# Optimization experiments

Hardware: AMD Instinct MI355X
Metric: run time of the kernel (lower is better)

The kernel has to match this reference:

```python
import jax, jax.numpy as jnp
import numpy as np

DROP_SCALE = 1e-4  # tf.multiply(feat_dropout, 0.0001)


def setup_inputs() -> dict:
    key = jax.random.key(0)
    k1, k2 = jax.random.split(key)
    B, C, N, D = 128, 2, 256, 256
    x = jax.random.normal(k1, (B, C, N, D), dtype=jnp.float32)
    # glorot_uniform for kernel [C*N*D, N]
    fan_in, fan_out = C * N * D, N
    limit = np.sqrt(6.0 / (fan_in + fan_out)).astype(np.float32)
    W = jax.random.uniform(k2, (fan_in, fan_out), dtype=jnp.float32,
                           minval=-limit, maxval=limit)
    return {"x": x, "W": W}


def _forward(x, W):
    B, C, N, D = x.shape
    K = N // 2  # with continuous data, exactly half strictly exceed the median
    # Keras Flatten(channels_first): permute to channels-last order, then flatten
    xf = jnp.transpose(x, (0, 2, 3, 1)).reshape(B, -1)          # [B, N*D*C]
    line = jax.nn.sigmoid(xf @ W)                                # [B, N]
    med = jnp.median(line, axis=-1, keepdims=True)               # [B, 1]
    mask = med < line                                            # [B, N] bool
    mask3 = jnp.broadcast_to(mask[:, None, :], (B, C, N))        # tile over channels
    # ragged boolean_mask + to_tensor == stable compaction of kept rows.
    # Stable argsort of (~mask) puts True (kept) positions first, in order.
    idx_att = jnp.argsort(~mask3, axis=-1, stable=True)[..., :K]   # [B, C, K]
    idx_drp = jnp.argsort(mask3, axis=-1, stable=True)[..., :K]    # [B, C, K]
    feat_att = jnp.take_along_axis(x, idx_att[..., None], axis=2)  # [B, C, K, D]
    feat_drp = jnp.take_along_axis(x, idx_drp[..., None], axis=2)  # [B, C, K, D]
    return feat_att + DROP_SCALE * feat_drp


def reference(x, W):
    return _forward(x, W)
```

## Files before the change

### kernel.cpp

```cpp
#include <hip/hip_runtime.h>

#define BATCH 128
#define CH    2
#define NN    256
#define DD    256
#define KTOT  131072
#define KHALF 128

#define KSPLIT 256
#define KLEN   (KTOT / KSPLIT)
#define KS     32
#define NSTAGE (KLEN / KS)
#define NTB    128
#define PITCH  40

typedef short bf16x8 __attribute__((ext_vector_type(8)));
typedef float f32x4  __attribute__((ext_vector_type(4)));

__device__ __forceinline__ unsigned short bf16_rne(float f) {
    unsigned int u = __float_as_uint(f);
    u += 0x7FFFu + ((u >> 16) & 1u);
    return (unsigned short)(u >> 16);
}
__device__ __forceinline__ float bf16f(unsigned short h) {
    return __uint_as_float(((unsigned int)h) << 16);
}
__device__ __forceinline__ uint4 pack8(const unsigned short* p) {
    uint4 r;
    r.x = (unsigned)p[0] | ((unsigned)p[1] << 16);
    r.y = (unsigned)p[2] | ((unsigned)p[3] << 16);
    r.z = (unsigned)p[4] | ((unsigned)p[5] << 16);
    r.w = (unsigned)p[6] | ((unsigned)p[7] << 16);
    return r;
}

template <bool ATOMIC>
__global__ __launch_bounds__(256, 2) void gemm_mfma(const float* __restrict__ x,
                                                    const float* __restrict__ W,
                                                    float* __restrict__ zout) {
    __shared__ unsigned short Ah[128][PITCH], Al[128][PITCH];
    __shared__ unsigned short Bh[NTB][PITCH], Bl[NTB][PITCH];

    const int bid = blockIdx.x;
    const int s   = ((bid >> 4) << 3) | (bid & 7);
    const int nh  = (bid >> 3) & 1;

    const int t  = threadIdx.x;
    const int k0 = s * KLEN;
    const int c  = k0 >> 16;
    const int nd_base = k0 & 65535;

    const int ra = t & 127;
    const int ha = t >> 7;
    const int cb = t & 127;
    const int hb = t >> 7;

    float av[16], bv[16];

    auto load_stage = [&](int st) {
        const float* xp = &x[(size_t)ra * KTOT + k0 + st * KS + 16 * ha];
        *(float4*)&av[0]  = *(const float4*)&xp[0];
        *(float4*)&av[4]  = *(const float4*)&xp[4];
        *(float4*)&av[8]  = *(const float4*)&xp[8];
        *(float4*)&av[12] = *(const float4*)&xp[12];
        const int nd0 = nd_base + st * KS + 16 * hb;
        const float* wp = &W[(size_t)(2 * nd0 + c) * NN + nh * NTB + cb];
#pragma unroll
        for (int i = 0; i < 16; ++i)
            bv[i] = wp[(size_t)i * 2 * NN];
    };

    auto write_stage = [&]() {
        unsigned short h[16], l[16];
#pragma unroll
        for (int i = 0; i < 16; ++i) {
            h[i] = bf16_rne(av[i]);
            l[i] = bf16_rne(av[i] - bf16f(h[i]));
        }
        *(uint4*)&Ah[ra][16 * ha]     = pack8(h);
        *(uint4*)&Ah[ra][16 * ha + 8] = pack8(h + 8);
        *(uint4*)&Al[ra][16 * ha]     = pack8(l);
        *(uint4*)&Al[ra][16 * ha + 8] = pack8(l + 8);
#pragma unroll
        for (int i = 0; i < 16; ++i) {
            h[i] = bf16_rne(bv[i]);
            l[i] = bf16_rne(bv[i] - bf16f(h[i]));
        }
        *(uint4*)&Bh[cb][16 * hb]     = pack8(h);
        *(uint4*)&Bh[cb][16 * hb + 8] = pack8(h + 8);
        *(uint4*)&Bl[cb][16 * hb]     = pack8(l);
        *(uint4*)&Bl[cb][16 * hb + 8] = pack8(l + 8);
    };

    const int lane = t & 63;
    const int wid  = t >> 6;
    const int wm   = (wid >> 1) * 64;
    const int wn   = (wid & 1) * 64;
    const int lr   = lane & 15;
    const int kq   = (lane >> 4) * 8;

    f32x4 acc[4][4] = {};

    auto compute_stage = [&]() {
        bf16x8 a_h[4], a_l[4];
#pragma unroll
        for (int mt = 0; mt < 4; ++mt) {
            a_h[mt] = *(const bf16x8*)&Ah[wm + mt * 16 + lr][kq];
            a_l[mt] = *(const bf16x8*)&Al[wm + mt * 16 + lr][kq];
        }
#pragma unroll
        for (int nt = 0; nt < 4; ++nt) {
            bf16x8 b_h = *(const bf16x8*)&Bh[wn + nt * 16 + lr][kq];
            bf16x8 b_l = *(const bf16x8*)&Bl[wn + nt * 16 + lr][kq];
#pragma unroll
            for (int mt = 0; mt < 4; ++mt) {
                acc[mt][nt] = __builtin_amdgcn_mfma_f32_16x16x32_bf16(a_h[mt], b_h, acc[mt][nt], 0, 0, 0);
                acc[mt][nt] = __builtin_amdgcn_mfma_f32_16x16x32_bf16(a_h[mt], b_l, acc[mt][nt], 0, 0, 0);
                acc[mt][nt] = __builtin_amdgcn_mfma_f32_16x16x32_bf16(a_l[mt], b_h, acc[mt][nt], 0, 0, 0);
            }
        }
    };

    load_stage(0);
    for (int st = 0; st < NSTAGE; ++st) {
        __syncthreads();
        write_stage();
        __syncthreads();
        if (st + 1 < NSTAGE) load_stage(st + 1);
        compute_stage();
    }

#pragma unroll
    for (int mt = 0; mt < 4; ++mt)
#pragma unroll
        for (int nt = 0; nt < 4; ++nt)
#pragma unroll
            for (int r = 0; r < 4; ++r) {
                const int row = wm + mt * 16 + (lane >> 4) * 4 + r;
                const int col = nh * NTB + wn + nt * 16 + lr;
                if (ATOMIC) atomicAdd(&zout[row * NN + col], acc[mt][nt][r]);
                else zout[(size_t)s * (BATCH * NN) + row * NN + col] = acc[mt][nt][r];
            }
}

__global__ __launch_bounds__(256) void reduce1(const float* __restrict__ part,
                                               float* __restrict__ part2) {
    const int g = blockIdx.x & 7;
    const int b = blockIdx.x >> 3;
    const int j = threadIdx.x;
    float v = 0.0f;
#pragma unroll
    for (int i = 0; i < 32; ++i)
        v += part[(size_t)(g * 32 + i) * (BATCH * NN) + b * NN + j];
    part2[(size_t)g * (BATCH * NN) + b * NN + j] = v;
}

__global__ __launch_bounds__(256) void select_kernel(const float* __restrict__ p2, int ngroups,
                                                     int* __restrict__ idx_att,
                                                     int* __restrict__ idx_drp) {
    __shared__ float zv[NN];
    __shared__ int   flags[NN];
    const int b = blockIdx.x;
    const int j = threadIdx.x;
    float v = 0.0f;
    for (int g = 0; g < ngroups; ++g)
        v += p2[(size_t)g * (BATCH * NN) + b * NN + j];
    zv[j] = v;
    __syncthreads();
    int rank = 0;
    for (int i = 0; i < NN; ++i) {
        const float u = zv[i];
        rank += (u < v) || (u == v && i < j);
    }
    const int kept = (rank >= KHALF) ? 1 : 0;
    flags[j] = kept;
    __syncthreads();
    int pos = 0;
    for (int i = 0; i < j; ++i) pos += flags[i];
    if (kept) idx_att[b * KHALF + pos]       = j;
    else      idx_drp[b * KHALF + (j - pos)] = j;
}

__global__ __launch_bounds__(256) void gather_kernel(const float* __restrict__ x,
                                                     const int* __restrict__ idx_att,
                                                     const int* __restrict__ idx_drp,
                                                     float* __restrict__ out) {
    const int row  = blockIdx.x * 4 + (threadIdx.x >> 6);
    const int lane = threadIdx.x & 63;
    const int k = row & 127;
    const int c = (row >> 7) & 1;
    const int b = row >> 8;
    const int ia = idx_att[b * KHALF + k];
    const int id = idx_drp[b * KHALF + k];
    const float4* pa = (const float4*)&x[((b * 2 + c) * NN + ia) * DD];
    const float4* pd = (const float4*)&x[((b * 2 + c) * NN + id) * DD];
    float4* po = (float4*)&out[(size_t)row * DD];
    const float4 a  = pa[lane];
    const float4 d4 = pd[lane];
    float4 o;
    o.x = a.x + 1e-4f * d4.x;
    o.y = a.y + 1e-4f * d4.y;
    o.z = a.z + 1e-4f * d4.z;
    o.w = a.w + 1e-4f * d4.w;
    po[lane] = o;
}

extern "C" void kernel_launch(void* const* d_in, const int* in_sizes, int n_in,
                              void* d_out, int out_size, void* d_ws, size_t ws_size,
                              hipStream_t stream) {
    const float* x = (const float*)d_in[0];
    const float* W = (const float*)d_in[1];
    float* out = (float*)d_out;

    const size_t part_bytes  = (size_t)KSPLIT * BATCH * NN * sizeof(float);
    const size_t part2_bytes = (size_t)8 * BATCH * NN * sizeof(float);
    const size_t idx_bytes   = (size_t)BATCH * KHALF * sizeof(int);

    if (ws_size >= part_bytes + part2_bytes + 2 * idx_bytes) {
        float* part    = (float*)d_ws;
        float* part2   = (float*)((char*)d_ws + part_bytes);
        int*   idx_att = (int*)((char*)d_ws + part_bytes + part2_bytes);
        int*   idx_drp = idx_att + BATCH * KHALF;
        gemm_mfma<false><<<512, 256, 0, stream>>>(x, W, part);
        reduce1<<<1024, 256, 0, stream>>>(part, part2);
        select_kernel<<<BATCH, 256, 0, stream>>>(part2, 8, idx_att, idx_drp);
        gather_kernel<<<BATCH * CH * KHALF / 4, 256, 0, stream>>>(x, idx_att, idx_drp, out);
    } else {
        float* z       = (float*)d_ws;
        int*   idx_att = (int*)((char*)d_ws + (size_t)BATCH * NN * sizeof(float));
        int*   idx_drp = idx_att + BATCH * KHALF;
        hipMemsetAsync(z, 0, (size_t)BATCH * NN * sizeof(float), stream);
        gemm_mfma<true><<<512, 256, 0, stream>>>(x, W, z);
        select_kernel<<<BATCH, 256, 0, stream>>>(z, 1, idx_att, idx_drp);
        gather_kernel<<<BATCH * CH * KHALF / 4, 256, 0, stream>>>(x, idx_att, idx_drp, out);
    }
}
```

Measured before the change: 274.6 us.

## Double split-K slices, double-buffer register prefetch, and use bf16 intrinsics

Templates the split-K GEMM on slice count and launches 512 slices (1024 blocks) when the workspace is large enough, keeping a 256-slice fallback. It adds a two-register-set prefetch with an unrolled stage loop so the next stage's global load is issued earlier. It also remaps block indices so neighbouring blocks take different slices, and uses packed bf16 conversion intrinsics for the hi/lo split. The extra parallelism costs twice the partial-sum traffic and more reduction work, and the two register sets raise register pressure.

```diff
diff --git a/kernel.cpp b/kernel.cpp
--- a/kernel.cpp
+++ b/kernel.cpp
@@ -1,4 +1,5 @@
 #include <hip/hip_runtime.h>
+#include <hip/hip_bf16.h>
 
 #define BATCH 128
 #define CH    2
@@ -7,43 +8,37 @@
 #define KTOT  131072
 #define KHALF 128
 
-#define KSPLIT 256
-#define KLEN   (KTOT / KSPLIT)
-#define KS     32
-#define NSTAGE (KLEN / KS)
-#define NTB    128
-#define PITCH  40
+#define KS    32
+#define NTB   128
+#define PITCH 40
 
 typedef short bf16x8 __attribute__((ext_vector_type(8)));
 typedef float f32x4  __attribute__((ext_vector_type(4)));
 
-__device__ __forceinline__ unsigned short bf16_rne(float f) {
-    unsigned int u = __float_as_uint(f);
-    u += 0x7FFFu + ((u >> 16) & 1u);
-    return (unsigned short)(u >> 16);
-}
-__device__ __forceinline__ float bf16f(unsigned short h) {
-    return __uint_as_float(((unsigned int)h) << 16);
-}
-__device__ __forceinline__ uint4 pack8(const unsigned short* p) {
-    uint4 r;
-    r.x = (unsigned)p[0] | ((unsigned)p[1] << 16);
-    r.y = (unsigned)p[2] | ((unsigned)p[3] << 16);
-    r.z = (unsigned)p[4] | ((unsigned)p[5] << 16);
-    r.w = (unsigned)p[6] | ((unsigned)p[7] << 16);
-    return r;
-}
-
-template <bool ATOMIC>
+__device__ __forceinline__ void hilo2(float a, float b, unsigned& hp, unsigned& lp) {
+    union { __hip_bfloat162 v; unsigned u; } H, L;
+    H.v = __float22bfloat162_rn(float2{a, b});
+    hp = H.u;
+    float2 hf = __bfloat1622float2(H.v);
+    L.v = __float22bfloat162_rn(float2{a - hf.x, b - hf.y});
+    lp = L.u;
+}
+
+template <int SLICES, bool ATOMIC>
 __global__ __launch_bounds__(256, 2) void gemm_mfma(const float* __restrict__ x,
                                                     const float* __restrict__ W,
                                                     float* __restrict__ zout) {
+    constexpr int KLEN = KTOT / SLICES;
+    constexpr int NST  = KLEN / KS;
+    constexpr int NBLK = SLICES * 2;
+
     __shared__ unsigned short Ah[128][PITCH], Al[128][PITCH];
     __shared__ unsigned short Bh[NTB][PITCH], Bl[NTB][PITCH];
 
-    const int bid = blockIdx.x;
-    const int s   = ((bid >> 4) << 3) | (bid & 7);
-    const int nh  = (bid >> 3) & 1;
+    const int bid     = blockIdx.x;
+    const int logical = (bid & 7) * (NBLK >> 3) + (bid >> 3);
+    const int s       = logical >> 1;
+    const int nh      = logical & 1;
 
     const int t  = threadIdx.x;
     const int k0 = s * KLEN;
@@ -55,41 +50,39 @@
     const int cb = t & 127;
     const int hb = t >> 7;
 
-    float av[16], bv[16];
-
-    auto load_stage = [&](int st) {
-        const float* xp = &x[(size_t)ra * KTOT + k0 + st * KS + 16 * ha];
+    const float* xrow = &x[(size_t)ra * KTOT + k0 + 16 * ha];
+    const float* wcol = &W[(size_t)(2 * (nd_base + 16 * hb) + c) * NN + nh * NTB + cb];
+
+    auto loadr = [&](float* av, float* bv, int st) {
+        const float* xp = xrow + st * KS;
         *(float4*)&av[0]  = *(const float4*)&xp[0];
         *(float4*)&av[4]  = *(const float4*)&xp[4];
         *(float4*)&av[8]  = *(const float4*)&xp[8];
         *(float4*)&av[12] = *(const float4*)&xp[12];
-        const int nd0 = nd_base + st * KS + 16 * hb;
-        const float* wp = &W[(size_t)(2 * nd0 + c) * NN + nh * NTB + cb];
+        const float* wp = wcol + (size_t)st * KS * 2 * NN;
 #pragma unroll
         for (int i = 0; i < 16; ++i)
             bv[i] = wp[(size_t)i * 2 * NN];
     };
 
-    auto write_stage = [&]() {
-        unsigned short h[16], l[16];
-#pragma unroll
-        for (int i = 0; i < 16; ++i) {
-            h[i] = bf16_rne(av[i]);
-            l[i] = bf16_rne(av[i] - bf16f(h[i]));
-        }
-        *(uint4*)&Ah[ra][16 * ha]     = pack8(h);
-        *(uint4*)&Ah[ra][16 * ha + 8] = pack8(h + 8);
-        *(uint4*)&Al[ra][16 * ha]     = pack8(l);
-        *(uint4*)&Al[ra][16 * ha + 8] = pack8(l + 8);
-#pragma unroll
-        for (int i = 0; i < 16; ++i) {
-            h[i] = bf16_rne(bv[i]);
-            l[i] = bf16_rne(bv[i] - bf16f(h[i]));
-        }
-        *(uint4*)&Bh[cb][16 * hb]     = pack8(h);
-        *(uint4*)&Bh[cb][16 * hb + 8] = pack8(h + 8);
-        *(uint4*)&Bl[cb][16 * hb]     = pack8(l);
-        *(uint4*)&Bl[cb][16 * hb + 8] = pack8(l + 8);
+    auto writest = [&](const float* av, const float* bv) {
+        uint4 H0, H1, L0, L1;
+        hilo2(av[0],  av[1],  H0.x, L0.x); hilo2(av[2],  av[3],  H0.y, L0.y);
+        hilo2(av[4],  av[5],  H0.z, L0.z); hilo2(av[6],  av[7],  H0.w, L0.w);
+        hilo2(av[8],  av[9],  H1.x, L1.x); hilo2(av[10], av[11], H1.y, L1.y);
+        hilo2(av[12], av[13], H1.z, L1.z); hilo2(av[14], av[15], H1.w, L1.w);
+        *(uint4*)&Ah[ra][16 * ha]     = H0;
+        *(uint4*)&Ah[ra][16 * ha + 8] = H1;
+        *(uint4*)&Al[ra][16 * ha]     = L0;
+        *(uint4*)&Al[ra][16 * ha + 8] = L1;
+        hilo2(bv[0],  bv[1],  H0.x, L0.x); hilo2(bv[2],  bv[3],  H0.y, L0.y);
+        hilo2(bv[4],  bv[5],  H0.z, L0.z); hilo2(bv[6],  bv[7],  H0.w, L0.w);
+        hilo2(bv[8],  bv[9],  H1.x, L1.x); hilo2(bv[10], bv[11], H1.y, L1.y);
+        hilo2(bv[12], bv[13], H1.z, L1.z); hilo2(bv[14], bv[15], H1.w, L1.w);
+        *(uint4*)&Bh[cb][16 * hb]     = H0;
+        *(uint4*)&Bh[cb][16 * hb + 8] = H1;
+        *(uint4*)&Bl[cb][16 * hb]     = L0;
+        *(uint4*)&Bl[cb][16 * hb + 8] = L1;
     };
 
     const int lane = t & 63;
@@ -101,7 +94,7 @@
 
     f32x4 acc[4][4] = {};
 
-    auto compute_stage = [&]() {
+    auto compute = [&]() {
         bf16x8 a_h[4], a_l[4];
 #pragma unroll
         for (int mt = 0; mt < 4; ++mt) {
@@ -121,13 +114,20 @@
         }
     };
 
-    load_stage(0);
-    for (int st = 0; st < NSTAGE; ++st) {
-        __syncthreads();
-        write_stage();
-        __syncthreads();
-        if (st + 1 < NSTAGE) load_stage(st + 1);
-        compute_stage();
+    float avA[16], bvA[16], avB[16], bvB[16];
+    loadr(avA, bvA, 0);
+#pragma unroll
+    for (int st = 0; st < NST; st += 2) {
+        if (st + 1 < NST) loadr(avB, bvB, st + 1);
+        __syncthreads();
+        writest(avA, bvA);
+        __syncthreads();
+        compute();
+        if (st + 2 < NST) loadr(avA, bvA, st + 2);
+        __syncthreads();
+        writest(avB, bvB);
+        __syncthreads();
+        compute();
     }
 
 #pragma unroll
@@ -143,10 +143,12 @@
             }
 }
 
+template <int SLICES>
 __global__ __launch_bounds__(256) void reduce1(const float* __restrict__ part,
                                                float* __restrict__ part2) {
-    const int g = blockIdx.x & 7;
-    const int b = blockIdx.x >> 3;
+    constexpr int GROUPS = SLICES / 32;
+    const int g = blockIdx.x % GROUPS;
+    const int b = blockIdx.x / GROUPS;
     const int j = threadIdx.x;
     float v = 0.0f;
 #pragma unroll
@@ -212,25 +214,37 @@
     const float* W = (const float*)d_in[1];
     float* out = (float*)d_out;
 
-    const size_t part_bytes  = (size_t)KSPLIT * BATCH * NN * sizeof(float);
-    const size_t part2_bytes = (size_t)8 * BATCH * NN * sizeof(float);
-    const size_t idx_bytes   = (size_t)BATCH * KHALF * sizeof(int);
-
-    if (ws_size >= part_bytes + part2_bytes + 2 * idx_bytes) {
+    const size_t zrow   = (size_t)BATCH * NN * sizeof(float);
+    const size_t idxB   = (size_t)BATCH * KHALF * sizeof(int);
+    const size_t pA     = 512 * zrow;
+    const size_t p2A    = 16 * zrow;
+    const size_t pB     = 256 * zrow;
+    const size_t p2B    = 8 * zrow;
+
+    if (ws_size >= pA + p2A + 2 * idxB) {
         float* part    = (float*)d_ws;
-        float* part2   = (float*)((char*)d_ws + part_bytes);
-        int*   idx_att = (int*)((char*)d_ws + part_bytes + part2_bytes);
+        float* part2   = (float*)((char*)d_ws + pA);
+        int*   idx_att = (int*)((char*)d_ws + pA + p2A);
         int*   idx_drp = idx_att + BATCH * KHALF;
-        gemm_mfma<false><<<512, 256, 0, stream>>>(x, W, part);
-        reduce1<<<1024, 256, 0, stream>>>(part, part2);
+        gemm_mfma<512, false><<<1024, 256, 0, stream>>>(x, W, part);
+        reduce1<512><<<16 * BATCH, 256, 0, stream>>>(part, part2);
+        select_kernel<<<BATCH, 256, 0, stream>>>(part2, 16, idx_att, idx_drp);
+        gather_kernel<<<BATCH * CH * KHALF / 4, 256, 0, stream>>>(x, idx_att, idx_drp, out);
+    } else if (ws_size >= pB + p2B + 2 * idxB) {
+        float* part    = (float*)d_ws;
+        float* part2   = (float*)((char*)d_ws + pB);
+        int*   idx_att = (int*)((char*)d_ws + pB + p2B);
+        int*   idx_drp = idx_att + BATCH * KHALF;
+        gemm_mfma<256, false><<<512, 256, 0, stream>>>(x, W, part);
+        reduce1<256><<<8 * BATCH, 256, 0, stream>>>(part, part2);
         select_kernel<<<BATCH, 256, 0, stream>>>(part2, 8, idx_att, idx_drp);
         gather_kernel<<<BATCH * CH * KHALF / 4, 256, 0, stream>>>(x, idx_att, idx_drp, out);
     } else {
         float* z       = (float*)d_ws;
-        int*   idx_att = (int*)((char*)d_ws + (size_t)BATCH * NN * sizeof(float));
+        int*   idx_att = (int*)((char*)d_ws + zrow);
         int*   idx_drp = idx_att + BATCH * KHALF;
-        hipMemsetAsync(z, 0, (size_t)BATCH * NN * sizeof(float), stream);
-        gemm_mfma<true><<<512, 256, 0, stream>>>(x, W, z);
+        hipMemsetAsync(z, 0, zrow, stream);
+        gemm_mfma<512, true><<<1024, 256, 0, stream>>>(x, W, z);
         select_kernel<<<BATCH, 256, 0, stream>>>(z, 1, idx_att, idx_drp);
         gather_kernel<<<BATCH * CH * KHALF / 4, 256, 0, stream>>>(x, idx_att, idx_drp, out);
     }
```

Result: slower. 298.6 us (+8.7%).
